# Performance work log

Measured on AMD Instinct MI355X. Metric: run time of the kernel, lower is better.

## Reference

```python
import jax, jax.numpy as jnp
import numpy as np

EMB_DIM = 256
N_EMBED = 1024
BETA = 0.25


def setup_inputs() -> dict:
    key = jax.random.key(0)
    k1, k2 = jax.random.split(key)
    encoderout = jax.random.normal(k1, (32, EMB_DIM, 32, 32), dtype=jnp.float32)
    # embedding.weight.data.normal_(mean=0, std=1/n_embed)
    codebook = jax.random.normal(k2, (N_EMBED, EMB_DIM), dtype=jnp.float32) * (1.0 / N_EMBED)
    return {"encoderout": encoderout, "codebook": codebook}


def reference(encoderout, codebook):
    # NCHW -> NHWC
    x = jnp.transpose(encoderout, (0, 2, 3, 1))  # [B,H,W,D]
    flat = x.reshape(-1, EMB_DIM)                # [N,D]
    d2 = (jnp.sum(flat * flat, axis=1, keepdims=True)
          + jnp.sum(codebook * codebook, axis=1)[None, :]
          - 2.0 * flat @ codebook.T)             # [N,K]
    idx = jnp.argmin(d2, axis=1)                 # [N]
    quant = codebook[idx].reshape(x.shape)       # [B,H,W,D]
    codebook_loss = jnp.mean((quant - jax.lax.stop_gradient(x)) ** 2)
    commitment_loss = jnp.mean((x - jax.lax.stop_gradient(quant)) ** 2)
    loss = codebook_loss + BETA * commitment_loss
    # FAITHFUL to source bug: straight-through output is overwritten by the
    # input permuted back to NCHW, so out == encoderout.
    out = jnp.transpose(x, (0, 3, 1, 2))
    return (out, loss, codebook_loss, commitment_loss)
```

## Files before the change

### kernel.cpp

```cpp
#include <hip/hip_runtime.h>
#include <stdint.h>

typedef short s8v __attribute__((ext_vector_type(8)));
typedef float f4v __attribute__((ext_vector_type(4)));

#define EMB_DIM 256
#define HW      1024
#define NROWS   32768
#define NELEM   (NROWS * EMB_DIM)

#define PK_OFF   0u
#define CBN_OFF  524288u
#define PSQ_OFF  528384u
#define PSM_OFF  530432u
#define DONE_OFF 532480u
#define XPK_OFF  1048576u

__device__ __forceinline__ unsigned f2bf(float f) {
    union { float f; unsigned u; } c; c.f = f;
    unsigned u = c.u;
    return (u + 0x7FFFu + ((u >> 16) & 1u)) >> 16;
}

__global__ __launch_bounds__(256) void prep_cb(const float* __restrict__ cb,
                                               unsigned short* __restrict__ pk,
                                               float* __restrict__ cbn,
                                               unsigned* __restrict__ done) {
    int T = blockIdx.x, t = threadIdx.x;
    if (T == 0 && t == 0) *done = 0u;
    {
        int code = t >> 4, seg = t & 15;
        const float* src = cb + (size_t)(T * 16 + code) * EMB_DIM + seg * 16;
        float s2 = 0.f;
        #pragma unroll
        for (int k = 0; k < 4; ++k) {
            float4 v = *(const float4*)(src + 4 * k);
            s2 += v.x * v.x + v.y * v.y + v.z * v.z + v.w * v.w;
        }
        #pragma unroll
        for (int m = 1; m < 16; m <<= 1) s2 += __shfl_xor(s2, m, 64);
        if (seg == 0) cbn[T * 16 + code] = s2;
    }
    #pragma unroll
    for (int it = 0; it < 2; ++it) {
        int idx = t + 256 * it;
        int s = idx >> 6, l = idx & 63, G = l >> 4, ci = l & 15;
        const float* q = cb + (size_t)(T * 16 + ci) * EMB_DIM + 32 * s + 8 * G;
        float4 v0 = *(const float4*)(q);
        float4 v1 = *(const float4*)(q + 4);
        unsigned o0 = f2bf(v0.x) | (f2bf(v0.y) << 16);
        unsigned o1 = f2bf(v0.z) | (f2bf(v0.w) << 16);
        unsigned o2 = f2bf(v1.x) | (f2bf(v1.y) << 16);
        unsigned o3 = f2bf(v1.z) | (f2bf(v1.w) << 16);
        *(uint4*)((char*)pk + (size_t)T * 8192 + (size_t)idx * 16) =
            make_uint4(o0, o1, o2, o3);
    }
}

__global__ __launch_bounds__(256, 2) void copy_pack(const float* __restrict__ x,
                                                    float* __restrict__ out,
                                                    uint4* __restrict__ xpk,
                                                    float* __restrict__ psq) {
    __shared__ float smemf[2][64 * 69];
    __shared__ float red[4];

    int t = threadIdx.x, blk = blockIdx.x;
    int b = blk >> 4, p0 = (blk & 15) << 6;
    const float* xb = x   + (size_t)b * (EMB_DIM * HW) + p0;
    float*       ob = out + (size_t)b * (EMB_DIM * HW) + p0;

    int pq = t & 15, dd = t >> 4;

    f4v vv[16];
    #pragma unroll
    for (int kd = 0; kd < 4; ++kd)
        #pragma unroll
        for (int c2 = 0; c2 < 4; ++c2) {
            int dl = dd + 16 * c2;
            vv[kd * 4 + c2] = *(const f4v*)(xb + (size_t)(kd * 64 + dl) * HW + 4 * pq);
        }

    float sq = 0.f;
    for (int kd = 0; kd < 4; ++kd) {
        float* sbuf = smemf[kd & 1];
        #pragma unroll
        for (int c2 = 0; c2 < 4; ++c2) {
            int dl = dd + 16 * c2;
            f4v v = vv[kd * 4 + c2];
            *(f4v*)(ob + (size_t)(kd * 64 + dl) * HW + 4 * pq) = v;
            sq += v.x * v.x + v.y * v.y + v.z * v.z + v.w * v.w;
            float* dst = &sbuf[dl * 69 + 4 * pq];
            dst[0] = v.x; dst[1] = v.y; dst[2] = v.z; dst[3] = v.w;
        }
        __syncthreads();
        #pragma unroll
        for (int it = 0; it < 2; ++it) {
            int f = t + 256 * it;
            int fl = f & 63, sL = (f >> 6) & 1, R = f >> 7;
            int fG = fl >> 4, fci = fl & 15;
            const float* q = &sbuf[(32 * sL + 8 * fG) * 69 + 16 * R + fci];
            unsigned o0 = f2bf(q[0])   | (f2bf(q[69])  << 16);
            unsigned o1 = f2bf(q[138]) | (f2bf(q[207]) << 16);
            unsigned o2 = f2bf(q[276]) | (f2bf(q[345]) << 16);
            unsigned o3 = f2bf(q[414]) | (f2bf(q[483]) << 16);
            xpk[((size_t)(blk * 4 + R) * 8 + 2 * kd + sL) * 64 + fl] =
                make_uint4(o0, o1, o2, o3);
        }
    }

    #pragma unroll
    for (int m = 1; m < 64; m <<= 1) sq += __shfl_xor(sq, m, 64);
    if ((t & 63) == 0) red[t >> 6] = sq;
    __syncthreads();
    if (t == 0) psq[blk] = red[0] + red[1] + red[2] + red[3];
}

__global__ __launch_bounds__(256, 2) void vq_dist2(const uint4* __restrict__ xpk,
                                                   const unsigned short* __restrict__ pk,
                                                   const float* __restrict__ cbn,
                                                   const float* __restrict__ psq,
                                                   float* __restrict__ psm,
                                                   unsigned* __restrict__ done,
                                                   float* __restrict__ out) {
    __shared__ float mloc[4][64];
    __shared__ bool  lastf;
    __shared__ double dred[4];

    int t = threadIdx.x, blk = blockIdx.x;
    int l = t & 63, w = t >> 6;
    int G = l >> 4, ci = l & 15;

    s8v a[4][8];
    const uint4* pa = xpk + (size_t)blk * 2048 + l;
    #pragma unroll
    for (int R = 0; R < 4; ++R)
        #pragma unroll
        for (int s = 0; s < 8; ++s)
            a[R][s] = *(const s8v*)&pa[(R * 8 + s) * 64];

    int qbase = w * 16, off = blk & 15;
    float cvs[16];
    #pragma unroll
    for (int T = 0; T < 16; ++T) cvs[T] = cbn[(qbase + T) * 16 + ci];

    float mv[4][4];
    #pragma unroll
    for (int R = 0; R < 4; ++R)
        #pragma unroll
        for (int r = 0; r < 4; ++r) mv[R][r] = 1e30f;

    const char* lbase = (const char*)pk + (size_t)l * 16;
    #pragma unroll 2
    for (int i = 0; i < 16; ++i) {
        int tt = (off + i) & 15;
        const char* pt = lbase + (size_t)(qbase + tt) * 8192;
        f4v ac0 = {0.f,0.f,0.f,0.f}, ac1 = {0.f,0.f,0.f,0.f};
        f4v ac2 = {0.f,0.f,0.f,0.f}, ac3 = {0.f,0.f,0.f,0.f};
        #pragma unroll
        for (int s = 0; s < 8; ++s) {
            s8v bf = *(const s8v*)(pt + (size_t)s * 1024);
            ac0 = __builtin_amdgcn_mfma_f32_16x16x32_bf16(a[0][s], bf, ac0, 0, 0, 0);
            ac1 = __builtin_amdgcn_mfma_f32_16x16x32_bf16(a[1][s], bf, ac1, 0, 0, 0);
            ac2 = __builtin_amdgcn_mfma_f32_16x16x32_bf16(a[2][s], bf, ac2, 0, 0, 0);
            ac3 = __builtin_amdgcn_mfma_f32_16x16x32_bf16(a[3][s], bf, ac3, 0, 0, 0);
        }
        float cv = cvs[tt];
        #pragma unroll
        for (int r = 0; r < 4; ++r) {
            mv[0][r] = fminf(mv[0][r], cv - 2.f * ac0[r]);
            mv[1][r] = fminf(mv[1][r], cv - 2.f * ac1[r]);
            mv[2][r] = fminf(mv[2][r], cv - 2.f * ac2[r]);
            mv[3][r] = fminf(mv[3][r], cv - 2.f * ac3[r]);
        }
    }

    #pragma unroll
    for (int R = 0; R < 4; ++R)
        #pragma unroll
        for (int r = 0; r < 4; ++r) {
            float v = mv[R][r];
            #pragma unroll
            for (int m = 1; m < 16; m <<= 1) v = fminf(v, __shfl_xor(v, m, 64));
            mv[R][r] = v;
        }
    if (ci == 0) {
        #pragma unroll
        for (int R = 0; R < 4; ++R)
            #pragma unroll
            for (int r = 0; r < 4; ++r)
                mloc[w][16 * R + 4 * G + r] = mv[R][r];
    }
    __syncthreads();

    if (t < 64) {
        float m = fminf(fminf(mloc[0][t], mloc[1][t]),
                        fminf(mloc[2][t], mloc[3][t]));
        #pragma unroll
        for (int mm = 1; mm < 64; mm <<= 1) m += __shfl_xor(m, mm, 64);
        if (t == 0) {
            __hip_atomic_store(&psm[blk], m, __ATOMIC_RELAXED, __HIP_MEMORY_SCOPE_AGENT);
            __threadfence();
            unsigned old = __hip_atomic_fetch_add(done, 1u, __ATOMIC_RELAXED,
                                                  __HIP_MEMORY_SCOPE_AGENT);
            lastf = (old == 511u);
        }
    }
    __syncthreads();

    if (lastf) {
        __threadfence();
        double s = 0.0;
        #pragma unroll
        for (int h = 0; h < 2; ++h) {
            int idx = t + 256 * h;
            s += (double)__hip_atomic_load(&psm[idx], __ATOMIC_RELAXED, __HIP_MEMORY_SCOPE_AGENT)
               + (double)psq[idx];
        }
        #pragma unroll
        for (int m = 1; m < 64; m <<= 1) s += __shfl_xor(s, m, 64);
        if (l == 0) dred[w] = s;
        __syncthreads();
        if (t == 0) {
            double tot = dred[0] + dred[1] + dred[2] + dred[3];
            double cl = tot / (double)NELEM;
            out[NELEM + 0] = (float)(1.25 * cl);
            out[NELEM + 1] = (float)cl;
            out[NELEM + 2] = (float)cl;
        }
    }
}

extern "C" void kernel_launch(void* const* d_in, const int* in_sizes, int n_in,
                              void* d_out, int out_size, void* d_ws, size_t ws_size,
                              hipStream_t stream) {
    const float* enc = (const float*)d_in[0];
    const float* cb  = (const float*)d_in[1];
    float* out = (float*)d_out;

    unsigned short* pk = (unsigned short*)((char*)d_ws + PK_OFF);
    float* cbn  = (float*)((char*)d_ws + CBN_OFF);
    float* psq  = (float*)((char*)d_ws + PSQ_OFF);
    float* psm  = (float*)((char*)d_ws + PSM_OFF);
    unsigned* done = (unsigned*)((char*)d_ws + DONE_OFF);
    uint4* xpk  = (uint4*)((char*)d_ws + XPK_OFF);

    prep_cb<<<64, 256, 0, stream>>>(cb, pk, cbn, done);
    copy_pack<<<512, 256, 0, stream>>>(enc, out, xpk, psq);
    vq_dist2<<<512, 256, 0, stream>>>(xpk, pk, cbn, psq, psm, done, out);
}
```

Baseline: 119.7 us.

## Fuse input packing into distance kernel with LDS double-buffered codebook tiles

Merges the copy/pack kernel and the distance/argmin kernel into one. The packed bf16 activations now stay in shared memory instead of going through a global workspace. The codebook is streamed through a double-buffered LDS tile, with each wave owning 16 rows and covering all 1024 codes, replacing per-wave global loads of a codebook quarter. This removes a kernel launch and the global round trip of packed activations. The cost is a larger LDS footprint, which may reduce occupancy, and 32 barrier-synchronised codebook stages per block.

```diff
diff --git a/kernel.cpp b/kernel.cpp
--- a/kernel.cpp
+++ b/kernel.cpp
@@ -14,7 +14,6 @@
 #define PSQ_OFF  528384u
 #define PSM_OFF  530432u
 #define DONE_OFF 532480u
-#define XPK_OFF  1048576u
 
 __device__ __forceinline__ unsigned f2bf(float f) {
     union { float f; unsigned u; } c; c.f = f;
@@ -57,20 +56,30 @@
     }
 }
 
-__global__ __launch_bounds__(256, 2) void copy_pack(const float* __restrict__ x,
-                                                    float* __restrict__ out,
-                                                    uint4* __restrict__ xpk,
-                                                    float* __restrict__ psq) {
+__global__ __launch_bounds__(256, 2) void vq_fused(const float* __restrict__ x,
+                                                   float* __restrict__ out,
+                                                   const unsigned short* __restrict__ pk,
+                                                   const float* __restrict__ cbn,
+                                                   float* __restrict__ psq,
+                                                   float* __restrict__ psm,
+                                                   unsigned* __restrict__ done) {
     __shared__ float smemf[2][64 * 69];
+    __shared__ uint4 fragB[2048];
+    __shared__ float cbnlds[1024];
+    __shared__ float mloc[4][16];
     __shared__ float red[4];
+    __shared__ bool  lastf;
+    __shared__ double dred[4];
 
     int t = threadIdx.x, blk = blockIdx.x;
     int b = blk >> 4, p0 = (blk & 15) << 6;
     const float* xb = x   + (size_t)b * (EMB_DIM * HW) + p0;
     float*       ob = out + (size_t)b * (EMB_DIM * HW) + p0;
 
+    int l = t & 63, w = t >> 6;
+    int G = l >> 4, ci = l & 15;
+
     int pq = t & 15, dd = t >> 4;
-
     f4v vv[16];
     #pragma unroll
     for (int kd = 0; kd < 4; ++kd)
@@ -79,6 +88,8 @@
             int dl = dd + 16 * c2;
             vv[kd * 4 + c2] = *(const f4v*)(xb + (size_t)(kd * 64 + dl) * HW + 4 * pq);
         }
+    #pragma unroll
+    for (int i = 0; i < 4; ++i) cbnlds[t + 256 * i] = cbn[t + 256 * i];
 
     float sq = 0.f;
     for (int kd = 0; kd < 4; ++kd) {
@@ -103,102 +114,78 @@
             unsigned o1 = f2bf(q[138]) | (f2bf(q[207]) << 16);
             unsigned o2 = f2bf(q[276]) | (f2bf(q[345]) << 16);
             unsigned o3 = f2bf(q[414]) | (f2bf(q[483]) << 16);
-            xpk[((size_t)(blk * 4 + R) * 8 + 2 * kd + sL) * 64 + fl] =
-                make_uint4(o0, o1, o2, o3);
-        }
-    }
-
+            fragB[(R * 8 + 2 * kd + sL) * 64 + fl] = make_uint4(o0, o1, o2, o3);
+        }
+        __syncthreads();
+    }
     #pragma unroll
     for (int m = 1; m < 64; m <<= 1) sq += __shfl_xor(sq, m, 64);
-    if ((t & 63) == 0) red[t >> 6] = sq;
+    if (l == 0) red[w] = sq;
+
+    const uint4* pks = (const uint4*)pk;
+    uint4 rA[4];
+    #pragma unroll
+    for (int i = 0; i < 4; ++i) rA[i] = pks[0 * 1024 + i * 256 + t];
+
+    s8v a[8];
+    #pragma unroll
+    for (int s = 0; s < 8; ++s) a[s] = *(const s8v*)&fragB[(w * 8 + s) * 64 + l];
     __syncthreads();
-    if (t == 0) psq[blk] = red[0] + red[1] + red[2] + red[3];
-}
-
-__global__ __launch_bounds__(256, 2) void vq_dist2(const uint4* __restrict__ xpk,
-                                                   const unsigned short* __restrict__ pk,
-                                                   const float* __restrict__ cbn,
-                                                   const float* __restrict__ psq,
-                                                   float* __restrict__ psm,
-                                                   unsigned* __restrict__ done,
-                                                   float* __restrict__ out) {
-    __shared__ float mloc[4][64];
-    __shared__ bool  lastf;
-    __shared__ double dred[4];
-
-    int t = threadIdx.x, blk = blockIdx.x;
-    int l = t & 63, w = t >> 6;
-    int G = l >> 4, ci = l & 15;
-
-    s8v a[4][8];
-    const uint4* pa = xpk + (size_t)blk * 2048 + l;
-    #pragma unroll
-    for (int R = 0; R < 4; ++R)
-        #pragma unroll
-        for (int s = 0; s < 8; ++s)
-            a[R][s] = *(const s8v*)&pa[(R * 8 + s) * 64];
-
-    int qbase = w * 16, off = blk & 15;
-    float cvs[16];
-    #pragma unroll
-    for (int T = 0; T < 16; ++T) cvs[T] = cbn[(qbase + T) * 16 + ci];
-
-    float mv[4][4];
-    #pragma unroll
-    for (int R = 0; R < 4; ++R)
-        #pragma unroll
-        for (int r = 0; r < 4; ++r) mv[R][r] = 1e30f;
-
-    const char* lbase = (const char*)pk + (size_t)l * 16;
-    #pragma unroll 2
-    for (int i = 0; i < 16; ++i) {
-        int tt = (off + i) & 15;
-        const char* pt = lbase + (size_t)(qbase + tt) * 8192;
+
+    #pragma unroll
+    for (int i = 0; i < 4; ++i) fragB[i * 256 + t] = rA[i];
+    #pragma unroll
+    for (int i = 0; i < 4; ++i) rA[i] = pks[1 * 1024 + i * 256 + t];
+
+    float mv[4] = {1e30f, 1e30f, 1e30f, 1e30f};
+
+    for (int p = 0; p < 32; ++p) {
+        __syncthreads();
+        if (p < 31) {
+            int dh = ((p + 1) & 1) << 10;
+            #pragma unroll
+            for (int i = 0; i < 4; ++i) fragB[dh + i * 256 + t] = rA[i];
+            if (p < 30) {
+                #pragma unroll
+                for (int i = 0; i < 4; ++i) rA[i] = pks[(size_t)(p + 2) * 1024 + i * 256 + t];
+            }
+        }
+        const uint4* B0 = &fragB[(p & 1) << 10];
         f4v ac0 = {0.f,0.f,0.f,0.f}, ac1 = {0.f,0.f,0.f,0.f};
-        f4v ac2 = {0.f,0.f,0.f,0.f}, ac3 = {0.f,0.f,0.f,0.f};
         #pragma unroll
         for (int s = 0; s < 8; ++s) {
-            s8v bf = *(const s8v*)(pt + (size_t)s * 1024);
-            ac0 = __builtin_amdgcn_mfma_f32_16x16x32_bf16(a[0][s], bf, ac0, 0, 0, 0);
-            ac1 = __builtin_amdgcn_mfma_f32_16x16x32_bf16(a[1][s], bf, ac1, 0, 0, 0);
-            ac2 = __builtin_amdgcn_mfma_f32_16x16x32_bf16(a[2][s], bf, ac2, 0, 0, 0);
-            ac3 = __builtin_amdgcn_mfma_f32_16x16x32_bf16(a[3][s], bf, ac3, 0, 0, 0);
-        }
-        float cv = cvs[tt];
-        #pragma unroll
-        for (int r = 0; r < 4; ++r) {
-            mv[0][r] = fminf(mv[0][r], cv - 2.f * ac0[r]);
-            mv[1][r] = fminf(mv[1][r], cv - 2.f * ac1[r]);
-            mv[2][r] = fminf(mv[2][r], cv - 2.f * ac2[r]);
-            mv[3][r] = fminf(mv[3][r], cv - 2.f * ac3[r]);
-        }
-    }
-
-    #pragma unroll
-    for (int R = 0; R < 4; ++R)
-        #pragma unroll
-        for (int r = 0; r < 4; ++r) {
-            float v = mv[R][r];
-            #pragma unroll
-            for (int m = 1; m < 16; m <<= 1) v = fminf(v, __shfl_xor(v, m, 64));
-            mv[R][r] = v;
-        }
+            s8v b0 = *(const s8v*)&B0[s * 64 + l];
+            s8v b1 = *(const s8v*)&B0[512 + s * 64 + l];
+            ac0 = __builtin_amdgcn_mfma_f32_16x16x32_bf16(a[s], b0, ac0, 0, 0, 0);
+            ac1 = __builtin_amdgcn_mfma_f32_16x16x32_bf16(a[s], b1, ac1, 0, 0, 0);
+        }
+        float cv0 = cbnlds[(2 * p) * 16 + ci];
+        float cv1 = cbnlds[(2 * p + 1) * 16 + ci];
+        #pragma unroll
+        for (int r = 0; r < 4; ++r)
+            mv[r] = fminf(mv[r], fminf(cv0 - 2.f * ac0[r], cv1 - 2.f * ac1[r]));
+    }
+
+    #pragma unroll
+    for (int r = 0; r < 4; ++r) {
+        #pragma unroll
+        for (int m = 1; m < 16; m <<= 1)
+            mv[r] = fminf(mv[r], __shfl_xor(mv[r], m, 64));
+    }
     if (ci == 0) {
         #pragma unroll
-        for (int R = 0; R < 4; ++R)
-            #pragma unroll
-            for (int r = 0; r < 4; ++r)
-                mloc[w][16 * R + 4 * G + r] = mv[R][r];
+        for (int r = 0; r < 4; ++r) mloc[w][4 * G + r] = mv[r];
     }
     __syncthreads();
 
     if (t < 64) {
-        float m = fminf(fminf(mloc[0][t], mloc[1][t]),
-                        fminf(mloc[2][t], mloc[3][t]));
+        float m = mloc[t >> 4][t & 15];
         #pragma unroll
         for (int mm = 1; mm < 64; mm <<= 1) m += __shfl_xor(m, mm, 64);
         if (t == 0) {
             __hip_atomic_store(&psm[blk], m, __ATOMIC_RELAXED, __HIP_MEMORY_SCOPE_AGENT);
+            __hip_atomic_store(&psq[blk], red[0] + red[1] + red[2] + red[3],
+                               __ATOMIC_RELAXED, __HIP_MEMORY_SCOPE_AGENT);
             __threadfence();
             unsigned old = __hip_atomic_fetch_add(done, 1u, __ATOMIC_RELAXED,
                                                   __HIP_MEMORY_SCOPE_AGENT);
@@ -214,7 +201,7 @@
         for (int h = 0; h < 2; ++h) {
             int idx = t + 256 * h;
             s += (double)__hip_atomic_load(&psm[idx], __ATOMIC_RELAXED, __HIP_MEMORY_SCOPE_AGENT)
-               + (double)psq[idx];
+               + (double)__hip_atomic_load(&psq[idx], __ATOMIC_RELAXED, __HIP_MEMORY_SCOPE_AGENT);
         }
         #pragma unroll
         for (int m = 1; m < 64; m <<= 1) s += __shfl_xor(s, m, 64);
@@ -242,9 +229,7 @@
     float* psq  = (float*)((char*)d_ws + PSQ_OFF);
     float* psm  = (float*)((char*)d_ws + PSM_OFF);
     unsigned* done = (unsigned*)((char*)d_ws + DONE_OFF);
-    uint4* xpk  = (uint4*)((char*)d_ws + XPK_OFF);
 
     prep_cb<<<64, 256, 0, stream>>>(cb, pk, cbn, done);
-    copy_pack<<<512, 256, 0, stream>>>(enc, out, xpk, psq);
-    vq_dist2<<<512, 256, 0, stream>>>(xpk, pk, cbn, psq, psm, done, out);
-}
+    vq_fused<<<512, 256, 0, stream>>>(enc, out, pk, cbn, psq, psm, done);
+}
```

Measured after the change: 173.6 us. +45.0%, slower.
